# Performance work log

Hardware: AMD Instinct MI355X
Metric: run time of the kernel (lower is better)

Reference implementation:

```python
import jax, jax.numpy as jnp
import numpy as np

B, S, E = 2, 2048, 2048
HQ, HK, D = 32, 8, 64
G = HQ // HK  # GQA groups

def _rope(t, cos, sin):
    # t: [B,S,H,D]; cos/sin: [1,S,1,D/2]
    t1, t2 = jnp.split(t, 2, axis=-1)
    return jnp.concatenate([t1 * cos - t2 * sin, t2 * cos + t1 * sin], axis=-1)

def setup_inputs() -> dict:
    key = jax.random.key(0)
    ks = jax.random.split(key, 8)
    sc = 1.0 / np.sqrt(E)
    return {
        "x": jax.random.normal(ks[0], (B, S, E), jnp.float32),
        "rope_cos": jax.random.uniform(ks[1], (1, S, 1, D // 2), jnp.float32),
        "rope_sin": jax.random.uniform(ks[2], (1, S, 1, D // 2), jnp.float32),
        "attn_mask": jnp.zeros((1, 1, S, S), jnp.float32),
        "Wq": jax.random.normal(ks[3], (E, HQ, D), jnp.float32) * sc,
        "Wk": jax.random.normal(ks[4], (E, HK, D), jnp.float32) * sc,
        "Wv": jax.random.normal(ks[5], (E, HK, D), jnp.float32) * sc,
        "Wo": jax.random.normal(ks[6], (HQ, D, E), jnp.float32) * (1.0 / np.sqrt(HQ * D)),
    }

def reference(x, rope_cos, rope_sin, attn_mask, Wq, Wk, Wv, Wo):
    # QKV projections (LinearGeneral, no bias)
    q = jnp.einsum('bse,ehd->bshd', x, Wq)
    k = jnp.einsum('bse,ehd->bshd', x, Wk)
    v = jnp.einsum('bse,ehd->bshd', x, Wv)
    # inline RoPE on q and k
    q = _rope(q, rope_cos, rope_sin)
    k = _rope(k, rope_cos, rope_sin)
    # [B,H,S,D]
    q = jnp.transpose(q, (0, 2, 1, 3))
    k = jnp.transpose(k, (0, 2, 1, 3))
    v = jnp.transpose(v, (0, 2, 1, 3))
    # GQA repeat of k/v to full query-head count (faithful to jnp.repeat in source)
    k = jnp.repeat(k, G, axis=1)
    v = jnp.repeat(v, G, axis=1)
    # explicit scores (NOTE: source applies no 1/sqrt(d) scaling)
    w = jnp.einsum('bhqd,bhkd->bhqk', q, k) + attn_mask
    w = jax.nn.softmax(w, axis=-1)
    o = jnp.einsum('bhqk,bhkd->bhqd', w, v)
    o = jnp.transpose(o, (0, 2, 1, 3))  # [B,S,H,D]
    return jnp.einsum('bshd,hde->bse', o, Wo)
```

## Files before the change

### kernel.cpp

```cpp
#include <hip/hip_runtime.h>
#include <hip/hip_bf16.h>

typedef __bf16 bf16_t;
typedef __bf16 bfrag __attribute__((ext_vector_type(8)));
typedef float f4 __attribute__((ext_vector_type(4)));

#define S_LEN 2048
#define HQ_N 32
#define HK_N 8
#define D_DIM 64
#define LOG2E 1.4426950408889634f

__global__ __launch_bounds__(256) void cvt_bf16(
    const float* __restrict__ src, bf16_t* __restrict__ dst, int n)
{
    int i = (blockIdx.x * 256 + threadIdx.x) * 8;
    if (i >= n) return;
    f4 a = *(const f4*)(src + i);
    f4 b = *(const f4*)(src + i + 4);
    bf16_t o[8];
#pragma unroll
    for (int j = 0; j < 4; ++j) { o[j] = (bf16_t)a[j]; o[4 + j] = (bf16_t)b[j]; }
    *(uint4*)(dst + i) = *(uint4*)o;
}

__global__ __launch_bounds__(256) void transpose_cvt(
    const float* __restrict__ src, bf16_t* __restrict__ dst,
    int K, int N, int row_off)
{
    __shared__ float T[32][33];
    const int n0 = blockIdx.x * 32;
    const int k0 = blockIdx.y * 32;
    const int tx = threadIdx.x;
    const int ty = threadIdx.y;
#pragma unroll
    for (int i = 0; i < 4; ++i)
        T[ty + 8 * i][tx] = src[(size_t)(k0 + ty + 8 * i) * N + n0 + tx];
    __syncthreads();
#pragma unroll
    for (int i = 0; i < 4; ++i)
        dst[(size_t)(row_off + n0 + ty + 8 * i) * K + k0 + tx] =
            (bf16_t)T[tx][ty + 8 * i];
}

template<bool OUT_BF16>
__global__ __launch_bounds__(256) void gemm_bt(
    const bf16_t* __restrict__ A, const bf16_t* __restrict__ Bt,
    void* __restrict__ Cv, int M, int N, int K, int ldc)
{
    __shared__ bf16_t As[128][72];
    __shared__ bf16_t Bs[128][72];
    const int tid  = threadIdx.x;
    const int wave = tid >> 6;
    const int lane = tid & 63;
    const int lrow = lane & 15;
    const int quad = lane >> 4;
    const int wm   = (wave >> 1) * 64;
    const int wn   = (wave & 1) * 64;
    const int bm   = blockIdx.y * 128;
    const int bn   = blockIdx.x * 128;

    f4 acc[4][4];
#pragma unroll
    for (int i = 0; i < 4; ++i)
#pragma unroll
        for (int j = 0; j < 4; ++j)
            acc[i][j] = (f4){0.f, 0.f, 0.f, 0.f};

    const int sr = tid >> 2;
    const int sc = (tid & 3) * 16;

    for (int k0 = 0; k0 < K; k0 += 64) {
        uint4 a0 = *(const uint4*)(A  + (size_t)(bm + sr)      * K + k0 + sc);
        uint4 a1 = *(const uint4*)(A  + (size_t)(bm + sr)      * K + k0 + sc + 8);
        uint4 a2 = *(const uint4*)(A  + (size_t)(bm + sr + 64) * K + k0 + sc);
        uint4 a3 = *(const uint4*)(A  + (size_t)(bm + sr + 64) * K + k0 + sc + 8);
        uint4 b0 = *(const uint4*)(Bt + (size_t)(bn + sr)      * K + k0 + sc);
        uint4 b1 = *(const uint4*)(Bt + (size_t)(bn + sr)      * K + k0 + sc + 8);
        uint4 b2 = *(const uint4*)(Bt + (size_t)(bn + sr + 64) * K + k0 + sc);
        uint4 b3 = *(const uint4*)(Bt + (size_t)(bn + sr + 64) * K + k0 + sc + 8);
        __syncthreads();
        *(uint4*)(&As[sr][sc])          = a0;
        *(uint4*)(&As[sr][sc + 8])      = a1;
        *(uint4*)(&As[sr + 64][sc])     = a2;
        *(uint4*)(&As[sr + 64][sc + 8]) = a3;
        *(uint4*)(&Bs[sr][sc])          = b0;
        *(uint4*)(&Bs[sr][sc + 8])      = b1;
        *(uint4*)(&Bs[sr + 64][sc])     = b2;
        *(uint4*)(&Bs[sr + 64][sc + 8]) = b3;
        __syncthreads();

#pragma unroll
        for (int kc = 0; kc < 2; ++kc) {
            bfrag aF[4], bF[4];
#pragma unroll
            for (int i = 0; i < 4; ++i)
                aF[i] = *(const bfrag*)(&As[wm + i * 16 + lrow][kc * 32 + quad * 8]);
#pragma unroll
            for (int j = 0; j < 4; ++j)
                bF[j] = *(const bfrag*)(&Bs[wn + j * 16 + lrow][kc * 32 + quad * 8]);
#pragma unroll
            for (int i = 0; i < 4; ++i)
#pragma unroll
                for (int j = 0; j < 4; ++j)
                    acc[i][j] = __builtin_amdgcn_mfma_f32_16x16x32_bf16(
                        aF[i], bF[j], acc[i][j], 0, 0, 0);
        }
    }

#pragma unroll
    for (int i = 0; i < 4; ++i)
#pragma unroll
        for (int j = 0; j < 4; ++j)
#pragma unroll
            for (int r = 0; r < 4; ++r) {
                int row = bm + wm + i * 16 + quad * 4 + r;
                int col = bn + wn + j * 16 + lrow;
                if (OUT_BF16)
                    ((bf16_t*)Cv)[(size_t)row * ldc + col] = (bf16_t)acc[i][j][r];
                else
                    ((float*)Cv)[(size_t)row * ldc + col] = acc[i][j][r];
            }
}

__global__ __launch_bounds__(256) void rope_fused(
    bf16_t* __restrict__ t, const float* __restrict__ cs,
    const float* __restrict__ sn)
{
    int idx = blockIdx.x * 256 + threadIdx.x;
    int cidx = idx % 1280;
    int row  = idx / 1280;
    int s    = row & (S_LEN - 1);
    int col, d1;
    float scale;
    if (cidx < 1024) {
        d1 = cidx & 31;
        col = (cidx >> 5) * 64 + d1;
        scale = LOG2E;
    } else {
        int c2 = cidx - 1024;
        d1 = c2 & 31;
        col = 2048 + (c2 >> 5) * 64 + d1;
        scale = 1.0f;
    }
    size_t base = (size_t)row * 3072 + col;
    float t1 = (float)t[base];
    float t2 = (float)t[base + 32];
    float c  = cs[s * 32 + d1];
    float s_ = sn[s * 32 + d1];
    t[base]      = (bf16_t)((t1 * c - t2 * s_) * scale);
    t[base + 32] = (bf16_t)((t2 * c + t1 * s_) * scale);
}

__global__ __launch_bounds__(256) void attn_mfma(
    const bf16_t* __restrict__ qkv, const float* __restrict__ mask,
    bf16_t* __restrict__ o)
{
    __shared__ bf16_t Ks[64][72];
    __shared__ bf16_t Vt[64][72];
    __shared__ bf16_t Ps[128][72];

    const int tid  = threadIdx.x;
    const int wave = tid >> 6;
    const int lane = tid & 63;
    const int lrow = lane & 15;
    const int quad = lane >> 4;
    const int qt   = blockIdx.x;
    const int h    = blockIdx.y;
    const int b    = blockIdx.z;
    const int hk   = h >> 2;
    const int s0   = qt * 128;
    const int wrow = wave * 32;

    bfrag vOnes;
#pragma unroll
    for (int j = 0; j < 8; ++j) vOnes[j] = (lrow == 0) ? (bf16_t)1.0f : (bf16_t)0.0f;

    bfrag qf[2][2];
#pragma unroll
    for (int m = 0; m < 2; ++m) {
        const bf16_t* qsrc = qkv + (size_t)(b * S_LEN + s0 + wrow + m * 16 + lrow) * 3072 + h * 64;
#pragma unroll
        for (int c = 0; c < 2; ++c)
            qf[m][c] = *(const bfrag*)(qsrc + c * 32 + quad * 8);
    }

    const float* mrow[2];
#pragma unroll
    for (int m = 0; m < 2; ++m)
        mrow[m] = mask + (size_t)(s0 + wrow + m * 16 + lrow) * S_LEN + quad * 4;

    f4 oacc[2][4], lacc[2];
#pragma unroll
    for (int m = 0; m < 2; ++m) {
        lacc[m] = (f4){0.f, 0.f, 0.f, 0.f};
#pragma unroll
        for (int n = 0; n < 4; ++n) oacc[m][n] = (f4){0.f, 0.f, 0.f, 0.f};
    }

    const int skey = tid >> 2;
    const int sdc  = (tid & 3) * 16;
    const int vg   = tid >> 5;
    const int vp   = tid & 31;

    for (int kt = 0; kt < 32; ++kt) {
        const bf16_t* ksrc = qkv + (size_t)(b * S_LEN + kt * 64 + skey) * 3072 + 2048 + hk * 64 + sdc;
        uint4 k0 = *(const uint4*)(ksrc);
        uint4 k1 = *(const uint4*)(ksrc + 8);
        unsigned int vw[8];
#pragma unroll
        for (int kk = 0; kk < 8; ++kk)
            vw[kk] = *(const unsigned int*)(qkv + (size_t)(b * S_LEN + kt * 64 + vg * 8 + kk) * 3072
                                            + 2560 + hk * 64 + 2 * vp);
        __syncthreads();
        *(uint4*)(&Ks[skey][sdc])     = k0;
        *(uint4*)(&Ks[skey][sdc + 8]) = k1;
        {
            unsigned short lo[8], hi[8];
#pragma unroll
            for (int kk = 0; kk < 8; ++kk) { lo[kk] = vw[kk] & 0xffff; hi[kk] = vw[kk] >> 16; }
            *(uint4*)(&Vt[2 * vp][vg * 8])     = *(uint4*)lo;
            *(uint4*)(&Vt[2 * vp + 1][vg * 8]) = *(uint4*)hi;
        }
        __syncthreads();

        f4 mk[2][4];
#pragma unroll
        for (int m = 0; m < 2; ++m)
#pragma unroll
            for (int n = 0; n < 4; ++n)
                mk[m][n] = *(const f4*)(mrow[m] + kt * 64 + n * 16);

        bfrag kf[4][2];
#pragma unroll
        for (int n = 0; n < 4; ++n)
#pragma unroll
            for (int c = 0; c < 2; ++c)
                kf[n][c] = *(const bfrag*)(&Ks[n * 16 + lrow][c * 32 + quad * 8]);

        f4 sc[2][4];
#pragma unroll
        for (int m = 0; m < 2; ++m)
#pragma unroll
            for (int n = 0; n < 4; ++n) {
                f4 a = (f4){0.f, 0.f, 0.f, 0.f};
                a = __builtin_amdgcn_mfma_f32_16x16x32_bf16(kf[n][0], qf[m][0], a, 0, 0, 0);
                a = __builtin_amdgcn_mfma_f32_16x16x32_bf16(kf[n][1], qf[m][1], a, 0, 0, 0);
                sc[m][n] = a;
            }

#pragma unroll
        for (int m = 0; m < 2; ++m)
#pragma unroll
            for (int n = 0; n < 4; ++n) {
                bf16_t p4[4];
#pragma unroll
                for (int r = 0; r < 4; ++r)
                    p4[r] = (bf16_t)exp2f(fmaf(mk[m][n][r], LOG2E, sc[m][n][r]));
                *(uint2*)(&Ps[wrow + m * 16 + lrow][n * 16 + quad * 4]) = *(uint2*)p4;
            }

        bfrag pf[2][2], vf[4][2];
#pragma unroll
        for (int m = 0; m < 2; ++m)
#pragma unroll
            for (int c = 0; c < 2; ++c)
                pf[m][c] = *(const bfrag*)(&Ps[wrow + m * 16 + lrow][c * 32 + quad * 8]);
#pragma unroll
        for (int n = 0; n < 4; ++n)
#pragma unroll
            for (int c = 0; c < 2; ++c)
                vf[n][c] = *(const bfrag*)(&Vt[n * 16 + lrow][c * 32 + quad * 8]);
#pragma unroll
        for (int m = 0; m < 2; ++m) {
#pragma unroll
            for (int n = 0; n < 4; ++n) {
                oacc[m][n] = __builtin_amdgcn_mfma_f32_16x16x32_bf16(pf[m][0], vf[n][0], oacc[m][n], 0, 0, 0);
                oacc[m][n] = __builtin_amdgcn_mfma_f32_16x16x32_bf16(pf[m][1], vf[n][1], oacc[m][n], 0, 0, 0);
            }
            lacc[m] = __builtin_amdgcn_mfma_f32_16x16x32_bf16(pf[m][0], vOnes, lacc[m], 0, 0, 0);
            lacc[m] = __builtin_amdgcn_mfma_f32_16x16x32_bf16(pf[m][1], vOnes, lacc[m], 0, 0, 0);
        }
    }

#pragma unroll
    for (int m = 0; m < 2; ++m)
#pragma unroll
        for (int r = 0; r < 4; ++r) {
            float lv = __shfl(lacc[m][r], lane & 48, 64);
            float inv = 1.f / lv;
            int row = b * S_LEN + s0 + wrow + m * 16 + quad * 4 + r;
#pragma unroll
            for (int n = 0; n < 4; ++n)
                o[(size_t)row * 2048 + h * 64 + n * 16 + lrow] = (bf16_t)(oacc[m][n][r] * inv);
        }
}

extern "C" void kernel_launch(void* const* d_in, const int* in_sizes, int n_in,
                              void* d_out, int out_size, void* d_ws, size_t ws_size,
                              hipStream_t stream)
{
    const float* x    = (const float*)d_in[0];
    const float* rc   = (const float*)d_in[1];
    const float* rs   = (const float*)d_in[2];
    const float* mask = (const float*)d_in[3];
    const float* Wq   = (const float*)d_in[4];
    const float* Wk   = (const float*)d_in[5];
    const float* Wv   = (const float*)d_in[6];
    const float* Wo   = (const float*)d_in[7];
    float* out = (float*)d_out;

    char* ws = (char*)d_ws;
    bf16_t* qkv = (bf16_t*)(ws);
    bf16_t* xb  = (bf16_t*)(ws + (24u << 20));
    bf16_t* ob  = xb;
    bf16_t* Wt3 = (bf16_t*)(ws + (40u << 20));
    bf16_t* Wot = (bf16_t*)(ws + (52u << 20));

    const int M = 2 * S_LEN;
    dim3 blk(256);

    cvt_bf16<<<(M * 2048) / (256 * 8), blk, 0, stream>>>(x, xb, M * 2048);
    transpose_cvt<<<dim3(64, 64), dim3(32, 8), 0, stream>>>(Wq, Wt3, 2048, 2048, 0);
    transpose_cvt<<<dim3(16, 64), dim3(32, 8), 0, stream>>>(Wk, Wt3, 2048,  512, 2048);
    transpose_cvt<<<dim3(16, 64), dim3(32, 8), 0, stream>>>(Wv, Wt3, 2048,  512, 2560);
    transpose_cvt<<<dim3(64, 64), dim3(32, 8), 0, stream>>>(Wo, Wot, 2048, 2048, 0);

    gemm_bt<true><<<dim3(3072 / 128, M / 128), blk, 0, stream>>>(
        xb, Wt3, qkv, M, 3072, 2048, 3072);

    rope_fused<<<(M * 1280) / 256, blk, 0, stream>>>(qkv, rc, rs);

    attn_mfma<<<dim3(16, 32, 2), blk, 0, stream>>>(qkv, mask, ob);

    gemm_bt<false><<<dim3(2048 / 128, M / 128), blk, 0, stream>>>(
        ob, Wot, out, M, 2048, 2048, 2048);
}
```

Before: 450.8 us.

## Pre-transpose V globally and load K/V MFMA fragments directly from global memory

A new kernel writes V transposed into a per-(batch, kv-head) [D][S] buffer that reuses the Wt3 workspace region. The attention kernel then drops its shared-memory K/V staging and both per-tile __syncthreads, loading K and V MFMA fragments straight from global memory and relying on L2/L1 for reuse across the four query heads. This removes the LDS round trip and the scattered V transpose loads, but costs an extra launch and V read/write, plus redundant global loads per wave since the four waves no longer share a staged tile.

```diff
diff --git a/kernel.cpp b/kernel.cpp
--- a/kernel.cpp
+++ b/kernel.cpp
@@ -41,6 +41,30 @@
     for (int i = 0; i < 4; ++i)
         dst[(size_t)(row_off + n0 + ty + 8 * i) * K + k0 + tx] =
             (bf16_t)T[tx][ty + 8 * i];
+}
+
+__global__ __launch_bounds__(256) void transpose_v(
+    const bf16_t* __restrict__ qkv, bf16_t* __restrict__ Vtg)
+{
+    __shared__ bf16_t T[32][66];
+    const int s0 = blockIdx.x * 32;
+    const int bh = blockIdx.y;
+    const int b  = bh >> 3;
+    const int hk = bh & 7;
+    const int tx = threadIdx.x;
+    const int ty = threadIdx.y;
+#pragma unroll
+    for (int i = 0; i < 4; ++i) {
+        const bf16_t* src = qkv + (size_t)(b * S_LEN + s0 + ty + 8 * i) * 3072 + 2560 + hk * 64;
+        T[ty + 8 * i][tx]      = src[tx];
+        T[ty + 8 * i][tx + 32] = src[tx + 32];
+    }
+    __syncthreads();
+#pragma unroll
+    for (int i = 0; i < 8; ++i) {
+        int d = ty + 8 * i;
+        Vtg[(size_t)(bh * 64 + d) * S_LEN + s0 + tx] = T[tx][d];
+    }
 }
 
 template<bool OUT_BF16>
@@ -153,11 +177,9 @@
 }
 
 __global__ __launch_bounds__(256) void attn_mfma(
-    const bf16_t* __restrict__ qkv, const float* __restrict__ mask,
-    bf16_t* __restrict__ o)
-{
-    __shared__ bf16_t Ks[64][72];
-    __shared__ bf16_t Vt[64][72];
+    const bf16_t* __restrict__ qkv, const bf16_t* __restrict__ Vtg,
+    const float* __restrict__ mask, bf16_t* __restrict__ o)
+{
     __shared__ bf16_t Ps[128][72];
 
     const int tid  = threadIdx.x;
@@ -190,6 +212,9 @@
     for (int m = 0; m < 2; ++m)
         mrow[m] = mask + (size_t)(s0 + wrow + m * 16 + lrow) * S_LEN + quad * 4;
 
+    const bf16_t* kbase = qkv + (size_t)(b * S_LEN + lrow) * 3072 + 2048 + hk * 64 + quad * 8;
+    const bf16_t* vbase = Vtg + (size_t)((b * 8 + hk) * 64 + lrow) * S_LEN + quad * 8;
+
     f4 oacc[2][4], lacc[2];
 #pragma unroll
     for (int m = 0; m < 2; ++m) {
@@ -198,45 +223,27 @@
         for (int n = 0; n < 4; ++n) oacc[m][n] = (f4){0.f, 0.f, 0.f, 0.f};
     }
 
-    const int skey = tid >> 2;
-    const int sdc  = (tid & 3) * 16;
-    const int vg   = tid >> 5;
-    const int vp   = tid & 31;
-
     for (int kt = 0; kt < 32; ++kt) {
-        const bf16_t* ksrc = qkv + (size_t)(b * S_LEN + kt * 64 + skey) * 3072 + 2048 + hk * 64 + sdc;
-        uint4 k0 = *(const uint4*)(ksrc);
-        uint4 k1 = *(const uint4*)(ksrc + 8);
-        unsigned int vw[8];
-#pragma unroll
-        for (int kk = 0; kk < 8; ++kk)
-            vw[kk] = *(const unsigned int*)(qkv + (size_t)(b * S_LEN + kt * 64 + vg * 8 + kk) * 3072
-                                            + 2560 + hk * 64 + 2 * vp);
-        __syncthreads();
-        *(uint4*)(&Ks[skey][sdc])     = k0;
-        *(uint4*)(&Ks[skey][sdc + 8]) = k1;
-        {
-            unsigned short lo[8], hi[8];
-#pragma unroll
-            for (int kk = 0; kk < 8; ++kk) { lo[kk] = vw[kk] & 0xffff; hi[kk] = vw[kk] >> 16; }
-            *(uint4*)(&Vt[2 * vp][vg * 8])     = *(uint4*)lo;
-            *(uint4*)(&Vt[2 * vp + 1][vg * 8]) = *(uint4*)hi;
-        }
-        __syncthreads();
-
+        bfrag kf[4][2];
+#pragma unroll
+        for (int n = 0; n < 4; ++n) {
+            const bf16_t* kp = kbase + (size_t)(kt * 64 + n * 16) * 3072;
+            kf[n][0] = *(const bfrag*)(kp);
+            kf[n][1] = *(const bfrag*)(kp + 32);
+        }
+        bfrag vf[4][2];
+#pragma unroll
+        for (int n = 0; n < 4; ++n) {
+            const bf16_t* vp = vbase + (size_t)(n * 16) * S_LEN + kt * 64;
+            vf[n][0] = *(const bfrag*)(vp);
+            vf[n][1] = *(const bfrag*)(vp + 32);
+        }
         f4 mk[2][4];
 #pragma unroll
         for (int m = 0; m < 2; ++m)
 #pragma unroll
             for (int n = 0; n < 4; ++n)
                 mk[m][n] = *(const f4*)(mrow[m] + kt * 64 + n * 16);
-
-        bfrag kf[4][2];
-#pragma unroll
-        for (int n = 0; n < 4; ++n)
-#pragma unroll
-            for (int c = 0; c < 2; ++c)
-                kf[n][c] = *(const bfrag*)(&Ks[n * 16 + lrow][c * 32 + quad * 8]);
 
         f4 sc[2][4];
 #pragma unroll
@@ -260,17 +267,12 @@
                 *(uint2*)(&Ps[wrow + m * 16 + lrow][n * 16 + quad * 4]) = *(uint2*)p4;
             }
 
-        bfrag pf[2][2], vf[4][2];
+        bfrag pf[2][2];
 #pragma unroll
         for (int m = 0; m < 2; ++m)
 #pragma unroll
             for (int c = 0; c < 2; ++c)
                 pf[m][c] = *(const bfrag*)(&Ps[wrow + m * 16 + lrow][c * 32 + quad * 8]);
-#pragma unroll
-        for (int n = 0; n < 4; ++n)
-#pragma unroll
-            for (int c = 0; c < 2; ++c)
-                vf[n][c] = *(const bfrag*)(&Vt[n * 16 + lrow][c * 32 + quad * 8]);
 #pragma unroll
         for (int m = 0; m < 2; ++m) {
 #pragma unroll
@@ -315,6 +317,7 @@
     bf16_t* xb  = (bf16_t*)(ws + (24u << 20));
     bf16_t* ob  = xb;
     bf16_t* Wt3 = (bf16_t*)(ws + (40u << 20));
+    bf16_t* Vtg = (bf16_t*)(ws + (40u << 20));
     bf16_t* Wot = (bf16_t*)(ws + (52u << 20));
 
     const int M = 2 * S_LEN;
@@ -331,7 +334,9 @@
 
     rope_fused<<<(M * 1280) / 256, blk, 0, stream>>>(qkv, rc, rs);
 
-    attn_mfma<<<dim3(16, 32, 2), blk, 0, stream>>>(qkv, mask, ob);
+    transpose_v<<<dim3(64, 16), dim3(32, 8), 0, stream>>>(qkv, Vtg);
+
+    attn_mfma<<<dim3(16, 32, 2), blk, 0, stream>>>(qkv, Vtg, mask, ob);
 
     gemm_bt<false><<<dim3(2048 / 128, M / 128), blk, 0, stream>>>(
         ob, Wot, out, M, 2048, 2048, 2048);
```

Result: slower. 599.1 us (+32.9%).
